# Kernel tuning notes

Measured on AMD Instinct MI355X. Metric: run time of the kernel, lower is better.

Reference implementation:

```python
import jax, jax.numpy as jnp
import numpy as np


def setup_inputs() -> dict:
    key = jax.random.key(0)
    # [N, n, m]: batch, transform length (axis 1), columns
    x = jax.random.normal(key, (32, 1024, 512), dtype=jnp.float32)
    return {"x": x}


def reference(x):
    # Faithful port of idct_odd_case: IDCT-III via a length-2n complex IFFT
    # on a Hermitian-symmetric-style mirrored array, exactly as the TF code.
    N, n, m = x.shape
    k = jnp.arange(n, dtype=jnp.float32)
    # t[k] = sqrt(2n) * exp(i*pi*k/(2n)); t[0] scaled by extra sqrt(2)
    t = jnp.sqrt(2.0 * n) * jnp.exp(1j * k * (np.pi / (2.0 * n)))
    t = t.at[0].multiply(jnp.sqrt(2.0))
    W = t.astype(jnp.complex64)[None, :, None]           # [1, n, 1]
    xc = x.astype(jnp.complex64)
    yy_up = W * xc                                        # [N, n, m]
    # -i * W[1:n] * reverse(x[1:n]) along the transform axis
    yy_down = (-1j) * W[:, 1:, :] * xc[:, n - 1:0:-1, :]  # [N, n-1, m]
    yy_mid = jnp.zeros((N, 1, m), dtype=jnp.complex64)
    yy = jnp.concatenate([yy_up, yy_mid, yy_down], axis=1)  # [N, 2n, m]
    y = jnp.fft.ifft(yy, axis=1)                          # matlab_ifft: ifft on axis 1
    return jnp.real(y[:, :n, :]).astype(jnp.float32)
```

## Files before the change

### kernel.cpp

```cpp
#include <hip/hip_runtime.h>

typedef unsigned short u16;
typedef __attribute__((ext_vector_type(8))) __bf16 bf16x8;
typedef __attribute__((ext_vector_type(4))) float f32x4;

#define GLOAD_LDS16(g, l)                                                                     \
  __builtin_amdgcn_global_load_lds((const __attribute__((address_space(1))) unsigned int*)(g), \
                                   (__attribute__((address_space(3))) unsigned int*)(l), 16, 0, 0)

static __device__ __forceinline__ u16 f2bf(float f) {
  unsigned int u = __float_as_uint(f);
  u += 0x7fffu + ((u >> 16) & 1u);
  return (u16)(u >> 16);
}

#define BATCH 32
#define NN 1024
#define MM 512

static __device__ __forceinline__ int swz(int r) { return ((r >> 1) ^ ((r & 1) << 2)) & 7; }

__global__ void fill_g(u16* __restrict__ G) {
  int idx = blockIdx.x * 256 + threadIdx.x;
  int jt  = idx >> 16;
  int s   = (idx >> 12) & 15;
  int row = (idx >> 6) & 63;
  int pc  = (idx >> 3) & 7;
  int sub = idx & 7;
  int dc = pc ^ (row & 7);
  int j = jt * 64 + row;
  int k;
  if (dc < 4) k = 2 * (s * 32 + dc * 8 + sub);
  else        k = 2 * (s * 32 + (dc - 4) * 8 + sub) + 1;
  float v;
  if (k == 0) {
    v = 0.03125f;
  } else {
    int ph = (k * (2 * j + 1)) & 4095;
    v = 0.04419417382415922f * cosf((float)ph * 1.5339807878856412e-3f);
  }
  G[idx] = f2bf(v);
}

__global__ __launch_bounds__(256, 4) void gemm_idct(const u16* __restrict__ G,
                                                    const float* __restrict__ X,
                                                    float* __restrict__ C) {
  __shared__ __align__(16) u16 sA[3][4096];
  __shared__ __align__(16) u16 sX[4096];
  const int wg    = blockIdx.x;
  const int xcd   = wg & 7;
  const int local = wg >> 3;
  const int jt    = local & 7;
  const int pg    = xcd * 32 + (local >> 3);
  const int ct    = pg & 7;
  const int b     = pg >> 3;

  const int t = threadIdx.x;
  const int wave = t >> 6, lane = t & 63;
  const int wm = wave >> 1, wn = wave & 1;
  const int lhi = lane >> 4, llo = lane & 15;

  const u16* gA = G + (size_t)jt * 65536 + t * 8;
#define ISSUE_A(buf, s)                                                        \
  do {                                                                         \
    GLOAD_LDS16(gA + (s) * 4096,        &sA[buf][t * 8]);                      \
    GLOAD_LDS16(gA + (s) * 4096 + 2048, &sA[buf][2048 + t * 8]);               \
  } while (0)

  const int cx = t & 63;
  const int kq = t >> 6;
  const float* gX = X + ((size_t)b * NN + kq * 16) * MM + ct * 64 + cx;

#define LOAD_X(s, XR)                                                          \
  do {                                                                         \
    const float* p = gX + (size_t)(s) * 64 * MM;                               \
    _Pragma("unroll") for (int i = 0; i < 16; ++i)                             \
      XR[i] = p[(size_t)i * MM];                                               \
  } while (0)

#define WRITE_X(XR)                                                            \
  do {                                                                         \
    const int f = swz(cx);                                                     \
    bf16x8 e, o;                                                               \
    _Pragma("unroll") for (int m = 0; m < 8; ++m) {                            \
      e[m] = (__bf16)XR[2 * m];                                                \
      o[m] = (__bf16)XR[2 * m + 1];                                            \
    }                                                                          \
    *(bf16x8*)&sX[cx * 64 + ((kq ^ f) << 3)] = e;                              \
    *(bf16x8*)&sX[cx * 64 + (((4 + kq) ^ f) << 3)] = o;                        \
  } while (0)

  f32x4 accE[2][2] = {};
  f32x4 accO[2][2] = {};
  float xrA[16], xrB[16];

#define STEP(s, XR)                                                            \
  do {                                                                         \
    WRITE_X(XR);                                \
    if ((s) < 15)                                                              \
      asm volatile("s_waitcnt vmcnt(18) lgkmcnt(0)" ::: "memory");             \
    else                                                                       \
      asm volatile("s_waitcnt vmcnt(0) lgkmcnt(0)" ::: "memory");              \
    __builtin_amdgcn_sched_barrier(0);                                         \
    __builtin_amdgcn_s_barrier();       \
    __builtin_amdgcn_sched_barrier(0);                                         \
    if ((s) < 14) {                                                            \
      ISSUE_A((s + 2) % 3, (s) + 2);                                           \
      LOAD_X((s) + 2, XR);                                                     \
    }                                                                          \
    {                                                                          \
      const u16* lA = &sA[(s) % 3][0];                                         \
      bf16x8 fe[2], fo[2], fxe[2], fxo[2];                                     \
      _Pragma("unroll") for (int mf = 0; mf < 2; ++mf) {                       \
        const int ra = wm * 32 + mf * 16 + llo;                                \
        const int fa = ra & 7;                                                 \
        fe[mf] = *(const bf16x8*)&lA[ra * 64 + ((lhi ^ fa) << 3)];             \
        fo[mf] = *(const bf16x8*)&lA[ra * 64 + (((4 + lhi) ^ fa) << 3)];       \
      }                                                                        \
      _Pragma("unroll") for (int nf = 0; nf < 2; ++nf) {                       \
        const int rb = wn * 32 + nf * 16 + llo;                                \
        const int fb = swz(rb);                                                \
        fxe[nf] = *(const bf16x8*)&sX[rb * 64 + ((lhi ^ fb) << 3)];            \
        fxo[nf] = *(const bf16x8*)&sX[rb * 64 + (((4 + lhi) ^ fb) << 3)];      \
      }                                                                        \
      __builtin_amdgcn_s_setprio(1);                                           \
      _Pragma("unroll") for (int mf = 0; mf < 2; ++mf)                         \
        _Pragma("unroll") for (int nf = 0; nf < 2; ++nf)                       \
          accE[mf][nf] = __builtin_amdgcn_mfma_f32_16x16x32_bf16(              \
              fe[mf], fxe[nf], accE[mf][nf], 0, 0, 0);                         \
      _Pragma("unroll") for (int mf = 0; mf < 2; ++mf)                         \
        _Pragma("unroll") for (int nf = 0; nf < 2; ++nf)                       \
          accO[mf][nf] = __builtin_amdgcn_mfma_f32_16x16x32_bf16(              \
              fo[mf], fxo[nf], accO[mf][nf], 0, 0, 0);                         \
      __builtin_amdgcn_s_setprio(0);                                           \
    }                                                                          \
    __builtin_amdgcn_sched_barrier(0);                                         \
    __builtin_amdgcn_s_barrier();  \
    __builtin_amdgcn_sched_barrier(0);                                         \
  } while (0)

  LOAD_X(0, xrA);
  ISSUE_A(0, 0);
  LOAD_X(1, xrB);
  ISSUE_A(1, 1);

#pragma unroll
  for (int ss = 0; ss < 8; ++ss) {
    STEP(2 * ss,     xrA);
    STEP(2 * ss + 1, xrB);
  }

  float* Cb = C + (size_t)b * NN * MM;
  const int cbase = ct * 64 + wn * 32 + llo;
#pragma unroll
  for (int mf = 0; mf < 2; ++mf)
#pragma unroll
    for (int nf = 0; nf < 2; ++nf) {
      const int jh0 = jt * 64 + wm * 32 + mf * 16 + lhi * 4;
      const int c   = cbase + nf * 16;
#pragma unroll
      for (int r = 0; r < 4; ++r) {
        const float ye = accE[mf][nf][r];
        const float yo = accO[mf][nf][r];
        const int j = jh0 + r;
        Cb[(size_t)j * MM + c]            = ye + yo;
        Cb[(size_t)(NN - 1 - j) * MM + c] = ye - yo;
      }
    }
#undef ISSUE_A
#undef LOAD_X
#undef WRITE_X
#undef STEP
}

extern "C" void kernel_launch(void* const* d_in, const int* in_sizes, int n_in,
                              void* d_out, int out_size, void* d_ws, size_t ws_size,
                              hipStream_t stream) {
  const float* x = (const float*)d_in[0];
  float* out = (float*)d_out;
  u16* G = (u16*)d_ws;

  fill_g<<<dim3(2048), dim3(256), 0, stream>>>(G);
  gemm_idct<<<dim3(2048), dim3(256), 0, stream>>>(G, x, out);
}
```

Measured before the change: 50.40 us.

## Pre-swizzle DCT matrix into MFMA fragment order and load it directly from global

The fill kernel now writes the cosine matrix in per-wave MFMA fragment order, so each wave reads its A operands straight from global memory as contiguous 16-byte vectors and the shared-memory staging of A with its triple buffer is dropped. Workgroups double to 512 threads covering 128 output rows, with K steps of 128 split into two MFMA sub-steps, which halves the number of barrier rounds and of redundant X tile loads. The cost is that global A loads now sit directly on the MFMA critical path, and X prefetch is single-buffered, so latency hiding depends on occupancy.

```diff
diff --git a/kernel.cpp b/kernel.cpp
--- a/kernel.cpp
+++ b/kernel.cpp
@@ -3,10 +3,6 @@
 typedef unsigned short u16;
 typedef __attribute__((ext_vector_type(8))) __bf16 bf16x8;
 typedef __attribute__((ext_vector_type(4))) float f32x4;
-
-#define GLOAD_LDS16(g, l)                                                                     \
-  __builtin_amdgcn_global_load_lds((const __attribute__((address_space(1))) unsigned int*)(g), \
-                                   (__attribute__((address_space(3))) unsigned int*)(l), 16, 0, 0)
 
 static __device__ __forceinline__ u16 f2bf(float f) {
   unsigned int u = __float_as_uint(f);
@@ -22,16 +18,17 @@
 
 __global__ void fill_g(u16* __restrict__ G) {
   int idx = blockIdx.x * 256 + threadIdx.x;
-  int jt  = idx >> 16;
-  int s   = (idx >> 12) & 15;
-  int row = (idx >> 6) & 63;
-  int pc  = (idx >> 3) & 7;
-  int sub = idx & 7;
-  int dc = pc ^ (row & 7);
-  int j = jt * 64 + row;
-  int k;
-  if (dc < 4) k = 2 * (s * 32 + dc * 8 + sub);
-  else        k = 2 * (s * 32 + (dc - 4) * 8 + sub) + 1;
+  int sub  = idx & 7;
+  int lane = (idx >> 3) & 63;
+  int mf   = (idx >> 9) & 1;
+  int eo   = (idx >> 10) & 1;
+  int ks   = (idx >> 11) & 1;
+  int s    = (idx >> 12) & 7;
+  int wm   = (idx >> 15) & 3;
+  int jt   = (idx >> 17) & 3;
+  int j = jt * 128 + wm * 32 + mf * 16 + (lane & 15);
+  int p = s * 64 + (ks * 4 + (lane >> 4)) * 8 + sub;
+  int k = 2 * p + eo;
   float v;
   if (k == 0) {
     v = 0.03125f;
@@ -42,16 +39,15 @@
   G[idx] = f2bf(v);
 }
 
-__global__ __launch_bounds__(256, 4) void gemm_idct(const u16* __restrict__ G,
+__global__ __launch_bounds__(512, 4) void gemm_idct(const u16* __restrict__ G,
                                                     const float* __restrict__ X,
                                                     float* __restrict__ C) {
-  __shared__ __align__(16) u16 sA[3][4096];
-  __shared__ __align__(16) u16 sX[4096];
+  __shared__ __align__(16) u16 sX[8192];
   const int wg    = blockIdx.x;
   const int xcd   = wg & 7;
   const int local = wg >> 3;
-  const int jt    = local & 7;
-  const int pg    = xcd * 32 + (local >> 3);
+  const int jt    = local & 3;
+  const int pg    = xcd * 32 + (local >> 2);
   const int ct    = pg & 7;
   const int b     = pg >> 3;
 
@@ -60,95 +56,78 @@
   const int wm = wave >> 1, wn = wave & 1;
   const int lhi = lane >> 4, llo = lane & 15;
 
-  const u16* gA = G + (size_t)jt * 65536 + t * 8;
-#define ISSUE_A(buf, s)                                                        \
+  const u16* gAF = G + (size_t)(jt * 4 + wm) * 32768 + lane * 8;
+
+  const int cx = t & 63;
+  const int kw = t >> 6;
+  const float* gX = X + ((size_t)b * NN + kw * 16) * MM + ct * 64 + cx;
+
+  float xr[16];
+#define LOAD_X(s)                                                              \
   do {                                                                         \
-    GLOAD_LDS16(gA + (s) * 4096,        &sA[buf][t * 8]);                      \
-    GLOAD_LDS16(gA + (s) * 4096 + 2048, &sA[buf][2048 + t * 8]);               \
+    const float* p = gX + (size_t)(s) * 128 * MM;                              \
+    _Pragma("unroll") for (int i = 0; i < 16; ++i)                             \
+      xr[i] = p[(size_t)i * MM];                                               \
   } while (0)
 
-  const int cx = t & 63;
-  const int kq = t >> 6;
-  const float* gX = X + ((size_t)b * NN + kq * 16) * MM + ct * 64 + cx;
-
-#define LOAD_X(s, XR)                                                          \
-  do {                                                                         \
-    const float* p = gX + (size_t)(s) * 64 * MM;                               \
-    _Pragma("unroll") for (int i = 0; i < 16; ++i)                             \
-      XR[i] = p[(size_t)i * MM];                                               \
-  } while (0)
-
-#define WRITE_X(XR)                                                            \
+#define WRITE_X()                                                              \
   do {                                                                         \
     const int f = swz(cx);                                                     \
     bf16x8 e, o;                                                               \
-    _Pragma("unroll") for (int m = 0; m < 8; ++m) {                            \
-      e[m] = (__bf16)XR[2 * m];                                                \
-      o[m] = (__bf16)XR[2 * m + 1];                                            \
+    _Pragma("unroll") for (int i = 0; i < 8; ++i) {                            \
+      e[i] = (__bf16)xr[2 * i];                                                \
+      o[i] = (__bf16)xr[2 * i + 1];                                            \
     }                                                                          \
-    *(bf16x8*)&sX[cx * 64 + ((kq ^ f) << 3)] = e;                              \
-    *(bf16x8*)&sX[cx * 64 + (((4 + kq) ^ f) << 3)] = o;                        \
+    const int ch = kw ^ f;                                                     \
+    *(bf16x8*)&sX[cx * 128 + ch * 8] = e;                                      \
+    *(bf16x8*)&sX[cx * 128 + 64 + ch * 8] = o;                                 \
   } while (0)
 
   f32x4 accE[2][2] = {};
   f32x4 accO[2][2] = {};
-  float xrA[16], xrB[16];
 
-#define STEP(s, XR)                                                            \
+#define STEP(s)                                                                \
   do {                                                                         \
-    WRITE_X(XR);                                \
-    if ((s) < 15)                                                              \
-      asm volatile("s_waitcnt vmcnt(18) lgkmcnt(0)" ::: "memory");             \
-    else                                                                       \
-      asm volatile("s_waitcnt vmcnt(0) lgkmcnt(0)" ::: "memory");              \
+    WRITE_X();                                        \
+    asm volatile("s_waitcnt lgkmcnt(0)" ::: "memory");                         \
     __builtin_amdgcn_sched_barrier(0);                                         \
-    __builtin_amdgcn_s_barrier();       \
+    __builtin_amdgcn_s_barrier();                       \
     __builtin_amdgcn_sched_barrier(0);                                         \
-    if ((s) < 14) {                                                            \
-      ISSUE_A((s + 2) % 3, (s) + 2);                                           \
-      LOAD_X((s) + 2, XR);                                                     \
-    }                                                                          \
-    {                                                                          \
-      const u16* lA = &sA[(s) % 3][0];                                         \
-      bf16x8 fe[2], fo[2], fxe[2], fxo[2];                                     \
+    if ((s) < 7) LOAD_X((s) + 1);                                              \
+    bf16x8 fe[2][2], fo[2][2];                                   \
+    _Pragma("unroll") for (int ks = 0; ks < 2; ++ks)                           \
       _Pragma("unroll") for (int mf = 0; mf < 2; ++mf) {                       \
-        const int ra = wm * 32 + mf * 16 + llo;                                \
-        const int fa = ra & 7;                                                 \
-        fe[mf] = *(const bf16x8*)&lA[ra * 64 + ((lhi ^ fa) << 3)];             \
-        fo[mf] = *(const bf16x8*)&lA[ra * 64 + (((4 + lhi) ^ fa) << 3)];       \
+        fe[ks][mf] = *(const bf16x8*)(gAF + (s) * 4096 + ((ks * 2 + 0) * 2 + mf) * 512); \
+        fo[ks][mf] = *(const bf16x8*)(gAF + (s) * 4096 + ((ks * 2 + 1) * 2 + mf) * 512); \
       }                                                                        \
+    _Pragma("unroll") for (int ks = 0; ks < 2; ++ks) {                         \
+      bf16x8 fxe[2], fxo[2];                                                   \
       _Pragma("unroll") for (int nf = 0; nf < 2; ++nf) {                       \
         const int rb = wn * 32 + nf * 16 + llo;                                \
-        const int fb = swz(rb);                                                \
-        fxe[nf] = *(const bf16x8*)&sX[rb * 64 + ((lhi ^ fb) << 3)];            \
-        fxo[nf] = *(const bf16x8*)&sX[rb * 64 + (((4 + lhi) ^ fb) << 3)];      \
+        const int cb = ((ks * 4 + lhi) ^ swz(rb)) << 3;                        \
+        fxe[nf] = *(const bf16x8*)&sX[rb * 128 + cb];                          \
+        fxo[nf] = *(const bf16x8*)&sX[rb * 128 + 64 + cb];                     \
       }                                                                        \
       __builtin_amdgcn_s_setprio(1);                                           \
       _Pragma("unroll") for (int mf = 0; mf < 2; ++mf)                         \
         _Pragma("unroll") for (int nf = 0; nf < 2; ++nf)                       \
           accE[mf][nf] = __builtin_amdgcn_mfma_f32_16x16x32_bf16(              \
-              fe[mf], fxe[nf], accE[mf][nf], 0, 0, 0);                         \
+              fe[ks][mf], fxe[nf], accE[mf][nf], 0, 0, 0);                     \
       _Pragma("unroll") for (int mf = 0; mf < 2; ++mf)                         \
         _Pragma("unroll") for (int nf = 0; nf < 2; ++nf)                       \
           accO[mf][nf] = __builtin_amdgcn_mfma_f32_16x16x32_bf16(              \
-              fo[mf], fxo[nf], accO[mf][nf], 0, 0, 0);                         \
+              fo[ks][mf], fxo[nf], accO[mf][nf], 0, 0, 0);                     \
       __builtin_amdgcn_s_setprio(0);                                           \
     }                                                                          \
     __builtin_amdgcn_sched_barrier(0);                                         \
-    __builtin_amdgcn_s_barrier();  \
+    __builtin_amdgcn_s_barrier();       \
     __builtin_amdgcn_sched_barrier(0);                                         \
   } while (0)
 
-  LOAD_X(0, xrA);
-  ISSUE_A(0, 0);
-  LOAD_X(1, xrB);
-  ISSUE_A(1, 1);
+  LOAD_X(0);
 
-#pragma unroll
-  for (int ss = 0; ss < 8; ++ss) {
-    STEP(2 * ss,     xrA);
-    STEP(2 * ss + 1, xrB);
-  }
+  STEP(0); STEP(1); STEP(2); STEP(3);
+  STEP(4); STEP(5); STEP(6); STEP(7);
 
   float* Cb = C + (size_t)b * NN * MM;
   const int cbase = ct * 64 + wn * 32 + llo;
@@ -156,7 +135,7 @@
   for (int mf = 0; mf < 2; ++mf)
 #pragma unroll
     for (int nf = 0; nf < 2; ++nf) {
-      const int jh0 = jt * 64 + wm * 32 + mf * 16 + lhi * 4;
+      const int jh0 = jt * 128 + wm * 32 + mf * 16 + lhi * 4;
       const int c   = cbase + nf * 16;
 #pragma unroll
       for (int r = 0; r < 4; ++r) {
@@ -167,7 +146,6 @@
         Cb[(size_t)(NN - 1 - j) * MM + c] = ye - yo;
       }
     }
-#undef ISSUE_A
 #undef LOAD_X
 #undef WRITE_X
 #undef STEP
@@ -181,5 +159,5 @@
   u16* G = (u16*)d_ws;
 
   fill_g<<<dim3(2048), dim3(256), 0, stream>>>(G);
-  gemm_idct<<<dim3(2048), dim3(256), 0, stream>>>(G, x, out);
+  gemm_idct<<<dim3(1024), dim3(512), 0, stream>>>(G, x, out);
 }
```

Result: faster. 47.07 us (-6.6%).
